# Optimization experiments

Hardware: AMD Instinct MI355X
Metric: run time of the kernel (lower is better)

## Reference

```python
import jax, jax.numpy as jnp
import numpy as np
from jax import lax

EPS = 1e-5  # flax BatchNorm default epsilon


def _conv(x, w, b, padding='SAME'):
    y = lax.conv_general_dilated(x, w, (1, 1), padding,
                                 dimension_numbers=('NHWC', 'HWIO', 'NHWC'))
    return y + b


def _maxpool(x, window, strides):
    return lax.reduce_window(x, -jnp.inf, lax.max,
                             (1,) + window + (1,), (1,) + strides + (1,), 'SAME')


def _bn_train(x, scale, bias):
    # training-mode BatchNorm: batch statistics over N,H,W
    m = x.mean(axis=(0, 1, 2))
    v = x.var(axis=(0, 1, 2))
    return (x - m) * lax.rsqrt(v + EPS) * scale + bias


def _lstm(x, wx, wh, b, carry, reverse):
    # x: (B, T, D); flax LSTMCell gate order i, f, g, o; bias lives on the
    # hidden dense in flax but is an equivalent single additive term here.
    xs = jnp.swapaxes(x @ wx + b, 0, 1)  # (T, B, 4H), input GEMM hoisted out of scan

    def step(ch, xt):
        c, h = ch
        g = xt + h @ wh
        i, f, gg, o = jnp.split(g, 4, axis=-1)
        c = jax.nn.sigmoid(f) * c + jax.nn.sigmoid(i) * jnp.tanh(gg)
        h = jax.nn.sigmoid(o) * jnp.tanh(c)
        return (c, h), h

    carry, ys = lax.scan(step, carry, xs, reverse=reverse)
    return carry, jnp.swapaxes(ys, 0, 1)  # (B, T, H)


def _forward(x, conv1_w, conv1_b, conv2_w, conv2_b, conv3_w, conv3_b, bn1_s, bn1_b,
             conv4_w, conv4_b, bn2_s, bn2_b, conv5_w, conv5_b, bn3_s, bn3_b,
             conv6_w, conv6_b, bn4_s, bn4_b, conv7_w, conv7_b, bn5_s, bn5_b,
             wq, bq, wk, bk, wv, bv,
             l1f_wx, l1f_wh, l1f_b, l1r_wx, l1r_wh, l1r_b,
             l2f_wx, l2f_wh, l2f_b, l2r_wx, l2r_wh, l2r_b, wo, bo):
    x = jax.nn.relu(_conv(x, conv1_w, conv1_b))
    x = _maxpool(x, (2, 2), (2, 2))
    x = jax.nn.relu(_conv(x, conv2_w, conv2_b))
    x = _maxpool(x, (2, 2), (2, 2))
    x = jax.nn.relu(_bn_train(_conv(x, conv3_w, conv3_b), bn1_s, bn1_b))
    x = jax.nn.relu(_bn_train(_conv(x, conv4_w, conv4_b), bn2_s, bn2_b))
    x = _maxpool(x, (2, 2), (1, 2))
    x = jax.nn.relu(_bn_train(_conv(x, conv5_w, conv5_b), bn3_s, bn3_b))
    x = jax.nn.relu(_bn_train(_conv(x, conv6_w, conv6_b), bn4_s, bn4_b))
    x = _maxpool(x, (2, 2), (1, 2))
    x = jax.nn.relu(_bn_train(_conv(x, conv7_w, conv7_b, padding='VALID'), bn5_s, bn5_b))
    B = x.shape[0]
    x = x.reshape(B, x.shape[1], -1)  # (B, T=H', W'*512); seq axis is height
    q = x @ wq + bq
    k = x @ wk + bk
    v = x @ wv + bv
    qk = jax.nn.softmax(jnp.einsum('btk,bsk->bts', q, k) / 32.0, axis=-1)
    x = jnp.einsum('btk,bts->bsk', v, qk)
    # stack 1: reverse LSTM deliberately starts from forward's FINAL carry (as in source)
    carry = (jnp.zeros((B, 256), x.dtype), jnp.zeros((B, 256), x.dtype))
    carry, y1 = _lstm(x, l1f_wx, l1f_wh, l1f_b, carry, reverse=False)
    carry, y2 = _lstm(x, l1r_wx, l1r_wh, l1r_b, carry, reverse=True)
    x1 = jnp.concatenate([y1, y2], axis=-1)
    # stack 2
    carry = (jnp.zeros((B, 512), x.dtype), jnp.zeros((B, 512), x.dtype))
    carry, y2b = _lstm(x1, l2f_wx, l2f_wh, l2f_b, carry, reverse=False)
    carry, y3 = _lstm(x1, l2r_wx, l2r_wh, l2r_b, carry, reverse=True)
    x = jnp.concatenate([y3, y2b], axis=-1)
    return x @ wo + bo


def setup_inputs() -> dict:
    key = jax.random.key(0)
    ks = iter(jax.random.split(key, 64))

    def cw(kh, kw, ci, co):
        return jax.random.normal(next(ks), (kh, kw, ci, co), jnp.float32) / np.float32(np.sqrt(kh * kw * ci))

    def dw(i, o):
        return jax.random.normal(next(ks), (i, o), jnp.float32) / np.float32(np.sqrt(i))

    z = lambda *s: jnp.zeros(s, jnp.float32)
    ones = lambda *s: jnp.ones(s, jnp.float32)
    class_nums = 1000
    d_in = 15 * 512  # W'=15 after conv stack, 512 channels
    inp = {
        'x': jax.random.normal(next(ks), (32, 64, 256, 3), jnp.float32),
        'conv1_w': cw(3, 3, 3, 64), 'conv1_b': z(64),
        'conv2_w': cw(3, 3, 64, 128), 'conv2_b': z(128),
        'conv3_w': cw(3, 3, 128, 256), 'conv3_b': z(256), 'bn1_s': ones(256), 'bn1_b': z(256),
        'conv4_w': cw(3, 3, 256, 256), 'conv4_b': z(256), 'bn2_s': ones(256), 'bn2_b': z(256),
        'conv5_w': cw(3, 3, 256, 512), 'conv5_b': z(512), 'bn3_s': ones(512), 'bn3_b': z(512),
        'conv6_w': cw(3, 3, 512, 512), 'conv6_b': z(512), 'bn4_s': ones(512), 'bn4_b': z(512),
        'conv7_w': cw(2, 2, 512, 512), 'conv7_b': z(512), 'bn5_s': ones(512), 'bn5_b': z(512),
        'wq': dw(d_in, 512), 'bq': z(512),
        'wk': dw(d_in, 512), 'bk': z(512),
        'wv': dw(d_in, 512), 'bv': z(512),
        'l1f_wx': dw(512, 4 * 256), 'l1f_wh': dw(256, 4 * 256), 'l1f_b': z(4 * 256),
        'l1r_wx': dw(512, 4 * 256), 'l1r_wh': dw(256, 4 * 256), 'l1r_b': z(4 * 256),
        'l2f_wx': dw(512, 4 * 512), 'l2f_wh': dw(512, 4 * 512), 'l2f_b': z(4 * 512),
        'l2r_wx': dw(512, 4 * 512), 'l2r_wh': dw(512, 4 * 512), 'l2r_b': z(4 * 512),
        'wo': dw(1024, class_nums), 'bo': z(class_nums),
    }
    return inp


def reference(x, conv1_w, conv1_b, conv2_w, conv2_b, conv3_w, conv3_b, bn1_s, bn1_b,
              conv4_w, conv4_b, bn2_s, bn2_b, conv5_w, conv5_b, bn3_s, bn3_b,
              conv6_w, conv6_b, bn4_s, bn4_b, conv7_w, conv7_b, bn5_s, bn5_b,
              wq, bq, wk, bk, wv, bv,
              l1f_wx, l1f_wh, l1f_b, l1r_wx, l1r_wh, l1r_b,
              l2f_wx, l2f_wh, l2f_b, l2r_wx, l2r_wh, l2r_b, wo, bo):
    return _forward(x, conv1_w, conv1_b, conv2_w, conv2_b, conv3_w, conv3_b, bn1_s, bn1_b,
                    conv4_w, conv4_b, bn2_s, bn2_b, conv5_w, conv5_b, bn3_s, bn3_b,
                    conv6_w, conv6_b, bn4_s, bn4_b, conv7_w, conv7_b, bn5_s, bn5_b,
                    wq, bq, wk, bk, wv, bv,
                    l1f_wx, l1f_wh, l1f_b, l1r_wx, l1r_wh, l1r_b,
                    l2f_wx, l2f_wh, l2f_b, l2r_wx, l2r_wh, l2r_b, wo, bo)
```

## Files before the change

kernel.cpp:

```cpp
#include <hip/hip_runtime.h>
#include <math.h>

#define DIV_UP(a,b) (((a)+(b)-1)/(b))

typedef _Float16 half_t;
typedef _Float16 half8 __attribute__((ext_vector_type(8)));
typedef float f32x4 __attribute__((ext_vector_type(4)));

#define FLAG_RELU   1
#define FLAG_OUTF32 2
#define FLAG_SPLITK 4
#define FLAG_ATOMIC 8
#define FLAG_BNSUMS 16

#define GLDS16(src, dst) \
  __builtin_amdgcn_global_load_lds((const __attribute__((address_space(1))) void*)(src), \
                                   (__attribute__((address_space(3))) void*)(dst), 16, 0, 0)

__device__ __forceinline__ float fsig_(float x){ return 1.0f/(1.0f+__expf(-x)); }
__device__ __forceinline__ float ftanh_(float x){
  float ax = fabsf(x);
  float e = __expf(-2.0f*ax);
  float t = (1.0f - e)/(1.0f + e);
  return copysignf(t, x);
}

struct TpAll {
  const float* src[14];
  half_t* dst[14];
  int K[14];
  int N[14];
  int prefix[15];
};

__global__ __launch_bounds__(256) void transpose_cvt_all_kernel(TpAll a)
{
  __shared__ float tile[32][33];
  int bid = blockIdx.x;
  int z = 0;
  while (bid >= a.prefix[z+1]) ++z;
  int local = bid - a.prefix[z];
  const float* w = a.src[z];
  half_t* wT = a.dst[z];
  int K = a.K[z], N = a.N[z];
  int tilesX = (N + 31) >> 5;
  int nt = (local % tilesX) * 32;
  int kt = (local / tilesX) * 32;
  int tx = threadIdx.x & 31, ty = threadIdx.x >> 5;
  #pragma unroll
  for (int r = 0; r < 4; ++r) {
    int k = kt + ty + r*8, n = nt + tx;
    tile[ty + r*8][tx] = (k < K && n < N) ? w[(long)k*N + n] : 0.f;
  }
  __syncthreads();
  #pragma unroll
  for (int r = 0; r < 4; ++r) {
    int n = nt + ty + r*8, k = kt + tx;
    if (n < N && k < K) wT[(long)n*K + k] = (half_t)tile[tx][ty + r*8];
  }
}

__global__ __launch_bounds__(256) void conv1_kernel(
    const float* __restrict__ x, const float* __restrict__ w,
    const float* __restrict__ bias, half_t* __restrict__ out)
{
  __shared__ float xs[3][258*3];
  int nb = blockIdx.x;
  int n = nb >> 6, ho = nb & 63;
  int tid = threadIdx.x;
  int co = tid & 63;
  float wreg[27];
  #pragma unroll
  for (int k = 0; k < 27; ++k) wreg[k] = w[k*64 + co];
  float bco = bias[co];
  for (int i = tid; i < 3*258*3; i += 256) {
    int row = i / (258*3); int rem = i % (258*3);
    int col = rem / 3;     int ci  = rem % 3;
    int ih = ho - 1 + row; int iw = col - 1;
    float v = 0.f;
    if (ih >= 0 && ih < 64 && iw >= 0 && iw < 256)
      v = x[(((long)n*64 + ih)*256 + iw)*3 + ci];
    xs[row][col*3 + ci] = v;
  }
  __syncthreads();
  int wave = tid >> 6;
  for (int p = 0; p < 64; ++p) {
    int wo = wave*64 + p;
    float acc = bco;
    #pragma unroll
    for (int kh = 0; kh < 3; ++kh)
      #pragma unroll
      for (int kw = 0; kw < 3; ++kw)
        #pragma unroll
        for (int ci = 0; ci < 3; ++ci)
          acc = fmaf(xs[kh][(wo+kw)*3 + ci], wreg[(kh*3+kw)*3 + ci], acc);
    acc = fmaxf(acc, 0.f);
    out[(((long)n*64 + ho)*256 + wo)*64 + co] = (half_t)acc;
  }
}

struct GOut { const half_t* wT; const float* bias; void* out; };

__global__ __launch_bounds__(256) void mfma_conv_kernel(
    const half_t* __restrict__ x, GOut g0, GOut g1, GOut g2,
    const half_t* __restrict__ zbuf, float* __restrict__ bns,
    int N,int H,int W,int Ci,int Ho,int Wo,int Co,
    int KH,int KW,int padH,int padW,
    int M,int K,int flags,int splitS)
{
  GOut g;
  int ciBeg = 0, ciEnd = Ci;
  if (flags & FLAG_SPLITK) {
    g = g0;
    int span = Ci / splitS;
    ciBeg = blockIdx.z * span;
    ciEnd = ciBeg + span;
  } else {
    g = (blockIdx.z == 0) ? g0 : (blockIdx.z == 1 ? g1 : g2);
  }
  const half_t* __restrict__ wT = g.wT;
  __shared__ half_t As[128*64];
  __shared__ half_t Bs[128*64];
  int tid = threadIdx.x;
  int m0 = blockIdx.y*128, n0 = blockIdx.x*128;
  int wave = tid >> 6, lane = tid & 63;
  int l15 = lane & 15, quad = lane >> 4;
  int x7 = lane & 7;
  int wm = (wave & 1) * 64, wn = (wave >> 1) * 64;

  int rSub = tid >> 3;
  int colHalf = (((tid & 7) ^ (rSub & 7))) * 8;

  int ho_[4], wo_[4], ni_[4]; bool av_[4];
  #pragma unroll
  for (int i = 0; i < 4; ++i) {
    int m = m0 + i*32 + rSub;
    av_[i] = m < M;
    int mm = av_[i] ? m : 0;
    wo_[i] = mm % Wo; int t2 = mm / Wo;
    ho_[i] = t2 % Ho; ni_[i] = t2 / Ho;
  }
  const half_t* bBase[4];
  #pragma unroll
  for (int i = 0; i < 4; ++i) {
    int n = n0 + i*32 + rSub;
    bBase[i] = (n < Co) ? (wT + (long)n*K + colHalf) : nullptr;
  }

  int pch0 = ((quad)     ^ x7) * 8;
  int pch1 = ((4 + quad) ^ x7) * 8;

  f32x4 acc[4][4];
  #pragma unroll
  for (int i = 0; i < 4; ++i)
    #pragma unroll
    for (int j = 0; j < 4; ++j)
      acc[i][j] = (f32x4){0.f, 0.f, 0.f, 0.f};

  int kg = ciBeg;
  for (int kh = 0; kh < KH; ++kh) {
    for (int kw = 0; kw < KW; ++kw) {
      long aOff[4]; bool aval[4];
      #pragma unroll
      for (int i = 0; i < 4; ++i) {
        int ih = ho_[i] - padH + kh, iw = wo_[i] - padW + kw;
        bool ok = av_[i] && ih >= 0 && ih < H && iw >= 0 && iw < W;
        aval[i] = ok;
        aOff[i] = ok ? ((((long)ni_[i]*H + ih)*W + iw)*(long)Ci + colHalf) : 0;
      }
      for (int ci = ciBeg; ci < ciEnd; ci += 64, kg += 64) {
        #pragma unroll
        for (int i = 0; i < 4; ++i) {
          const half_t* sa = aval[i] ? (x + aOff[i] + ci) : zbuf;
          GLDS16(sa, As + i*2048 + wave*512);
          const half_t* sb = bBase[i] ? (bBase[i] + kg) : zbuf;
          GLDS16(sb, Bs + i*2048 + wave*512);
        }
        __syncthreads();
        {
          half8 af[4], bf[4];
          #pragma unroll
          for (int i = 0; i < 4; ++i)
            af[i] = *reinterpret_cast<half8*>(&As[(wm + i*16 + l15)*64 + pch0]);
          #pragma unroll
          for (int j = 0; j < 4; ++j)
            bf[j] = *reinterpret_cast<half8*>(&Bs[(wn + j*16 + l15)*64 + pch0]);
          #pragma unroll
          for (int i = 0; i < 4; ++i)
            #pragma unroll
            for (int j = 0; j < 4; ++j)
              acc[i][j] = __builtin_amdgcn_mfma_f32_16x16x32_f16(af[i], bf[j], acc[i][j], 0, 0, 0);
        }
        {
          half8 af[4], bf[4];
          #pragma unroll
          for (int i = 0; i < 4; ++i)
            af[i] = *reinterpret_cast<half8*>(&As[(wm + i*16 + l15)*64 + pch1]);
          #pragma unroll
          for (int j = 0; j < 4; ++j)
            bf[j] = *reinterpret_cast<half8*>(&Bs[(wn + j*16 + l15)*64 + pch1]);
          #pragma unroll
          for (int i = 0; i < 4; ++i)
            #pragma unroll
            for (int j = 0; j < 4; ++j)
              acc[i][j] = __builtin_amdgcn_mfma_f32_16x16x32_f16(af[i], bf[j], acc[i][j], 0, 0, 0);
        }
        __syncthreads();
      }
    }
  }

  if (flags & FLAG_BNSUMS) {
    float* red = (float*)As;
    #pragma unroll
    for (int j = 0; j < 4; ++j) {
      int n = n0 + wn + j*16 + l15;
      float bv = g.bias[n];
      float s = 0.f, q = 0.f;
      #pragma unroll
      for (int i = 0; i < 4; ++i)
        #pragma unroll
        for (int r = 0; r < 4; ++r) {
          int m = m0 + wm + i*16 + quad*4 + r;
          if (m < M) { float v = acc[i][j][r] + bv; s += v; q += v*v; }
        }
      int idx = ((((wave*4 + quad)*16 + l15)*4) + j)*2;
      red[idx] = s; red[idx+1] = q;
    }
    __syncthreads();
    if (tid < 128) {
      int hi = tid >> 6;
      int jj = (tid >> 4) & 3, ll = tid & 15;
      float s = 0.f, q = 0.f;
      #pragma unroll
      for (int w2 = 0; w2 < 2; ++w2)
        #pragma unroll
        for (int qd = 0; qd < 4; ++qd) {
          int idx = (((((hi*2 + w2)*4 + qd)*16 + ll)*4) + jj)*2;
          s += red[idx]; q += red[idx+1];
        }
      int n = n0 + tid;
      atomicAdd(&bns[n], s);
      atomicAdd(&bns[Co + n], q);
    }
  }

  #pragma unroll
  for (int i = 0; i < 4; ++i) {
    #pragma unroll
    for (int r = 0; r < 4; ++r) {
      int m = m0 + wm + i*16 + quad*4 + r;
      if (m >= M) continue;
      #pragma unroll
      for (int j = 0; j < 4; ++j) {
        int n = n0 + wn + j*16 + l15;
        if (n >= Co) continue;
        if (flags & FLAG_ATOMIC) {
          atomicAdd(&((float*)g.out)[(long)m*Co + n], acc[i][j][r]);
        } else {
          float v = acc[i][j][r] + g.bias[n];
          if (flags & FLAG_RELU) v = fmaxf(v, 0.f);
          if (flags & FLAG_OUTF32) ((float*)g.out)[(long)m*Co + n] = v;
          else ((half_t*)g.out)[(long)m*Co + n] = (half_t)v;
        }
      }
    }
  }
}

__global__ __launch_bounds__(256) void maxpool8_kernel(
    const half_t* __restrict__ x, half_t* __restrict__ out,
    int N,int H,int W,int C,int Ho,int Wo,int sH,int sW)
{
  int C8 = C >> 3;
  long idx = (long)blockIdx.x*256 + threadIdx.x;
  long total8 = (long)N*Ho*Wo*C8;
  if (idx >= total8) return;
  int cb = (int)(idx % C8);
  long pix = idx / C8;
  int wo = (int)(pix % Wo); long t2 = pix / Wo;
  int ho = (int)(t2 % Ho); int n = (int)(t2 / Ho);
  int c = cb * 8;
  float m[8];
  #pragma unroll
  for (int e = 0; e < 8; ++e) m[e] = -INFINITY;
  for (int i = 0; i < 2; ++i) {
    int ih = ho*sH + i;
    if (ih >= H) continue;
    for (int j = 0; j < 2; ++j) {
      int iw = wo*sW + j;
      if (iw >= W) continue;
      half8 v = *reinterpret_cast<const half8*>(x + (((long)n*H + ih)*W + iw)*C + c);
      #pragma unroll
      for (int e = 0; e < 8; ++e) m[e] = fmaxf(m[e], (float)v[e]);
    }
  }
  half8 o;
  #pragma unroll
  for (int e = 0; e < 8; ++e) o[e] = (half_t)m[e];
  *reinterpret_cast<half8*>(out + idx*8) = o;
}

__global__ __launch_bounds__(256) void bn_apply_relu8_kernel(
    half_t* __restrict__ x, const float* __restrict__ sums,
    const float* __restrict__ scale, const float* __restrict__ bias,
    long total8, int C, float invN)
{
  long idx = (long)blockIdx.x*256 + threadIdx.x;
  if (idx >= total8) return;
  int c = (int)((idx*8) % C);
  half8 v = *reinterpret_cast<half8*>(x + idx*8);
  half8 o;
  #pragma unroll
  for (int e = 0; e < 8; ++e) {
    float mean = sums[c+e] * invN;
    float var  = sums[C + c+e] * invN - mean*mean;
    float rstd = rsqrtf(var + 1e-5f);
    float y = ((float)v[e] - mean) * rstd * scale[c+e] + bias[c+e];
    o[e] = (half_t)fmaxf(y, 0.0f);
  }
  *reinterpret_cast<half8*>(x + idx*8) = o;
}

__global__ __launch_bounds__(256) void bn_pool8_kernel(
    const half_t* __restrict__ x, half_t* __restrict__ out,
    const float* __restrict__ sums, const float* __restrict__ scale,
    const float* __restrict__ bias,
    int N,int H,int W,int C,int Ho,int Wo,int sH,int sW, float invN)
{
  int C8 = C >> 3;
  long idx = (long)blockIdx.x*256 + threadIdx.x;
  long total8 = (long)N*Ho*Wo*C8;
  if (idx >= total8) return;
  int cb = (int)(idx % C8);
  long pix = idx / C8;
  int wo = (int)(pix % Wo); long t2 = pix / Wo;
  int ho = (int)(t2 % Ho); int n = (int)(t2 / Ho);
  int c = cb * 8;
  float mean[8], rs[8], bb[8];
  #pragma unroll
  for (int e = 0; e < 8; ++e) {
    mean[e] = sums[c+e] * invN;
    float var = sums[C + c+e] * invN - mean[e]*mean[e];
    rs[e] = rsqrtf(var + 1e-5f) * scale[c+e];
    bb[e] = bias[c+e];
  }
  float m[8];
  #pragma unroll
  for (int e = 0; e < 8; ++e) m[e] = -INFINITY;
  for (int i = 0; i < 2; ++i) {
    int ih = ho*sH + i;
    if (ih >= H) continue;
    for (int j = 0; j < 2; ++j) {
      int iw = wo*sW + j;
      if (iw >= W) continue;
      half8 v = *reinterpret_cast<const half8*>(x + (((long)n*H + ih)*W + iw)*C + c);
      #pragma unroll
      for (int e = 0; e < 8; ++e) {
        float y = fmaxf(((float)v[e] - mean[e]) * rs[e] + bb[e], 0.f);
        m[e] = fmaxf(m[e], y);
      }
    }
  }
  half8 o;
  #pragma unroll
  for (int e = 0; e < 8; ++e) o[e] = (half_t)m[e];
  *reinterpret_cast<half8*>(out + idx*8) = o;
}

__global__ __launch_bounds__(256) void bias_fill_kernel(
    float* __restrict__ out, const float* __restrict__ b0,
    const float* __restrict__ b1, const float* __restrict__ b2, int total)
{
  int idx = blockIdx.x*256 + threadIdx.x;
  if (idx >= total) return;
  int n = idx % 1536;
  float v = (n < 512) ? b0[n] : (n < 1024 ? b1[n-512] : b2[n-1024]);
  out[idx] = v;
}

__global__ __launch_bounds__(256) void attention_kernel(
    const float* __restrict__ qkv, half_t* __restrict__ out,
    int T, int D, int ld)
{
  int b = blockIdx.x;
  int tid = threadIdx.x;
  __shared__ float P[15][16];
  if (tid < T*T) {
    int t = tid / T, s = tid % T;
    const float* qp = qkv + ((long)b*T + t)*ld;
    const float* kp = qkv + ((long)b*T + s)*ld + 512;
    float acc = 0.f;
    for (int d = 0; d < D; d += 4) {
      float4 qv = *reinterpret_cast<const float4*>(qp + d);
      float4 kv = *reinterpret_cast<const float4*>(kp + d);
      acc += qv.x*kv.x + qv.y*kv.y + qv.z*kv.z + qv.w*kv.w;
    }
    P[t][s] = acc * (1.0f/32.0f);
  }
  __syncthreads();
  if (tid < T) {
    float mx = -INFINITY;
    for (int s = 0; s < T; ++s) mx = fmaxf(mx, P[tid][s]);
    float sum = 0.f;
    for (int s = 0; s < T; ++s) { float e = expf(P[tid][s] - mx); P[tid][s] = e; sum += e; }
    float inv = 1.0f / sum;
    for (int s = 0; s < T; ++s) P[tid][s] *= inv;
  }
  __syncthreads();
  for (int idx = tid; idx < T*D; idx += 256) {
    int s = idx / D, kk2 = idx % D;
    float acc = 0.f;
    #pragma unroll
    for (int t = 0; t < 15; ++t)
      acc += qkv[((long)b*T + t)*ld + 1024 + kk2] * P[t][s];
    out[((long)b*T + s)*D + kk2] = (half_t)acc;
  }
}

#define MAXK 512
#define HSROW (MAXK + 8)

template<int N64, int HLOG>
__device__ __forceinline__ void stage_h(
    const unsigned long long* __restrict__ src, half_t (*hs)[HSROW], int tid)
{
  unsigned long long tmp[N64];
  #pragma unroll
  for (int u = 0; u < N64; ++u)
    tmp[u] = __hip_atomic_load(src + tid + u*256, __ATOMIC_RELAXED, __HIP_MEMORY_SCOPE_AGENT);
  #pragma unroll
  for (int u = 0; u < N64; ++u) {
    int idx = tid + u*256;
    int row = idx >> (HLOG - 2);
    int col = (idx & ((1 << (HLOG - 2)) - 1)) * 4;
    *reinterpret_cast<unsigned long long*>(&hs[row][col]) = tmp[u];
  }
}

__global__ __launch_bounds__(256, 1) void lstm_persistent_kernel(
    const float* __restrict__ preF, const float* __restrict__ preR,
    const float* __restrict__ whF, const float* __restrict__ whR,
    half_t* __restrict__ hbuf, half_t* __restrict__ y,
    int* __restrict__ flags, int H, int nblk,
    int ystride, int yoffF, int yoffR)
{
  __shared__ half_t BsT[64][HSROW];
  __shared__ half_t hs[32][HSROW];
  __shared__ float gates[32][65];
  int tid = threadIdx.x;
  int jb0 = blockIdx.x * 16;
  int H4 = 4 * H;
  int lane = tid & 63, wave = tid >> 6;
  int l15 = lane & 15, quad = lane >> 4;
  int bb = tid >> 3;
  int jj0 = (tid & 7) * 2;

  float cst[2] = {0.f, 0.f};

  for (int idx = tid; idx < H*64; idx += 256) {
    int k = idx >> 6, c = idx & 63;
    int g = c >> 4, jj = c & 15;
    BsT[c][k] = (half_t)whF[(long)k*H4 + g*H + jb0 + jj];
  }
  const float* pre = preF;
  int yoff = yoffF;
  __syncthreads();

  for (int s = 0; s < 30; ++s) {
    if (s == 15) {
      __syncthreads();
      for (int idx = tid; idx < H*64; idx += 256) {
        int k = idx >> 6, c = idx & 63;
        int g = c >> 4, jj = c & 15;
        BsT[c][k] = (half_t)whR[(long)k*H4 + g*H + jb0 + jj];
      }
      pre = preR; yoff = yoffR;
      __syncthreads();
    }
    int t = (s < 15) ? s : 29 - s;

    float pv[8];
    {
      const float* pp = pre + (long)(bb*15 + t)*H4 + jb0 + jj0;
      #pragma unroll
      for (int p = 0; p < 2; ++p) {
        pv[p*4+0] = pp[p];
        pv[p*4+1] = pp[H + p];
        pv[p*4+2] = pp[2*H + p];
        pv[p*4+3] = pp[3*H + p];
      }
    }

    const unsigned long long* hsrc =
        (const unsigned long long*)(hbuf + (long)(s & 1) * 32 * H);
    if (H == 512) stage_h<16, 9>(hsrc, hs, tid);
    else          stage_h<8, 8>(hsrc, hs, tid);
    __syncthreads();

    f32x4 acc0 = {0.f,0.f,0.f,0.f}, acc1 = {0.f,0.f,0.f,0.f};
    for (int k0 = 0; k0 < H; k0 += 32) {
      half8 bf = *reinterpret_cast<half8*>(&BsT[wave*16 + l15][k0 + quad*8]);
      half8 a0 = *reinterpret_cast<half8*>(&hs[l15][k0 + quad*8]);
      half8 a1 = *reinterpret_cast<half8*>(&hs[16 + l15][k0 + quad*8]);
      acc0 = __builtin_amdgcn_mfma_f32_16x16x32_f16(a0, bf, acc0, 0, 0, 0);
      acc1 = __builtin_amdgcn_mfma_f32_16x16x32_f16(a1, bf, acc1, 0, 0, 0);
    }
    #pragma unroll
    for (int r = 0; r < 4; ++r) {
      gates[quad*4 + r][wave*16 + l15]      = acc0[r];
      gates[16 + quad*4 + r][wave*16 + l15] = acc1[r];
    }
    __syncthreads();

    unsigned hpack;
    {
      half_t hn2[2];
      #pragma unroll
      for (int p = 0; p < 2; ++p) {
        int jj = jj0 + p;
        float gi = pv[p*4+0] + gates[bb][jj];
        float gf = pv[p*4+1] + gates[bb][16 + jj];
        float gg = pv[p*4+2] + gates[bb][32 + jj];
        float go = pv[p*4+3] + gates[bb][48 + jj];
        gi = fsig_(gi); gf = fsig_(gf); gg = ftanh_(gg); go = fsig_(go);
        float cn = gf * cst[p] + gi * gg;
        cst[p] = cn;
        hn2[p] = (half_t)(go * ftanh_(cn));
      }
      hpack = *reinterpret_cast<unsigned*>(hn2);
      half_t* hdst = hbuf + (long)((s + 1) & 1) * 32 * H;
      __hip_atomic_store((unsigned*)(hdst + (long)bb*H + jb0 + jj0), hpack,
                         __ATOMIC_RELAXED, __HIP_MEMORY_SCOPE_AGENT);
    }

    if (s < 29) {
      __syncthreads();
      if (tid == 0)
        __hip_atomic_store(&flags[blockIdx.x*16], s + 1,
                           __ATOMIC_RELAXED, __HIP_MEMORY_SCOPE_AGENT);
      *reinterpret_cast<unsigned*>(&y[(long)(bb*15 + t)*ystride + yoff + jb0 + jj0]) = hpack;
      if (tid < 64) {
        int target = s + 1;
        for (;;) {
          int vv = (tid < nblk)
            ? __hip_atomic_load(&flags[tid*16], __ATOMIC_RELAXED, __HIP_MEMORY_SCOPE_AGENT)
            : target;
          if (__all(vv >= target)) break;
          __builtin_amdgcn_s_sleep(1);
        }
      }
      __syncthreads();
    } else {
      *reinterpret_cast<unsigned*>(&y[(long)(bb*15 + t)*ystride + yoff + jb0 + jj0]) = hpack;
    }
  }
}

extern "C" void kernel_launch(void* const* d_in, const int* in_sizes, int n_in,
                              void* d_out, int out_size, void* d_ws, size_t ws_size,
                              hipStream_t stream)
{
  const float* x       = (const float*)d_in[0];
  const float* c1w     = (const float*)d_in[1];  const float* c1b = (const float*)d_in[2];
  const float* c2w     = (const float*)d_in[3];  const float* c2b = (const float*)d_in[4];
  const float* c3w     = (const float*)d_in[5];  const float* c3b = (const float*)d_in[6];
  const float* bn1s    = (const float*)d_in[7];  const float* bn1b = (const float*)d_in[8];
  const float* c4w     = (const float*)d_in[9];  const float* c4b = (const float*)d_in[10];
  const float* bn2s    = (const float*)d_in[11]; const float* bn2b = (const float*)d_in[12];
  const float* c5w     = (const float*)d_in[13]; const float* c5b = (const float*)d_in[14];
  const float* bn3s    = (const float*)d_in[15]; const float* bn3b = (const float*)d_in[16];
  const float* c6w     = (const float*)d_in[17]; const float* c6b = (const float*)d_in[18];
  const float* bn4s    = (const float*)d_in[19]; const float* bn4b = (const float*)d_in[20];
  const float* c7w     = (const float*)d_in[21]; const float* c7b = (const float*)d_in[22];
  const float* bn5s    = (const float*)d_in[23]; const float* bn5b = (const float*)d_in[24];
  const float* wq      = (const float*)d_in[25]; const float* bq = (const float*)d_in[26];
  const float* wk      = (const float*)d_in[27]; const float* bk = (const float*)d_in[28];
  const float* wv      = (const float*)d_in[29]; const float* bv = (const float*)d_in[30];
  const float* l1f_wx  = (const float*)d_in[31]; const float* l1f_wh = (const float*)d_in[32]; const float* l1f_b = (const float*)d_in[33];
  const float* l1r_wx  = (const float*)d_in[34]; const float* l1r_wh = (const float*)d_in[35]; const float* l1r_b = (const float*)d_in[36];
  const float* l2f_wx  = (const float*)d_in[37]; const float* l2f_wh = (const float*)d_in[38]; const float* l2f_b = (const float*)d_in[39];
  const float* l2r_wx  = (const float*)d_in[40]; const float* l2r_wh = (const float*)d_in[41]; const float* l2r_b = (const float*)d_in[42];
  const float* wo      = (const float*)d_in[43]; const float* bo = (const float*)d_in[44];
  float* outp = (float*)d_out;

  char* base = (char*)d_ws;
  half_t* actA = (half_t*)base;
  half_t* actB = (half_t*)(base + 67108864);
  half_t* wtA  = (half_t*)(base + 100663296);
  float*  f32a = (float*)(base + 143687680);
  half_t* h16a = (half_t*)(base + 158736384);

  half_t* wt2  = wtA;
  half_t* wt3  = wtA + 73728;
  half_t* wt4  = wtA + 368640;
  half_t* wt5  = wtA + 958464;
  half_t* wt6  = wtA + 2138112;
  half_t* wt7  = wtA + 4497408;
  half_t* wtq  = wtA + 5545984;
  half_t* wtk  = wtA + 9478144;
  half_t* wtv  = wtA + 13410304;
  half_t* wt1f = wtA + 17342464;
  half_t* wt1r = wtA + 17866752;
  half_t* wt2f = wtA + 18391040;
  half_t* wt2r = wtA + 19439616;
  half_t* wto  = wtA + 20488192;

  float* qkvbuf = f32a;
  float* pre1f = f32a + 737280;
  float* pre1r = f32a + 1228800;
  float* pre2f = f32a + 1720320;
  float* pre2r = f32a + 2703360;

  half_t* ao  = h16a;
  half_t* x1  = h16a + 245760;
  half_t* x2  = h16a + 491520;
  half_t* hb1 = h16a + 983040;
  half_t* hb2 = hb1 + 16384;
  int*    flags1 = (int*)(hb2 + 32768);
  int*    flags2 = flags1 + 512;
  half_t* zbuf   = (half_t*)(flags2 + 512);
  float*  bnz    = (float*)(zbuf + 32);

  auto convm = [&](const half_t* in, const half_t* wt, const float* b, void* out,
                   int N,int H,int W,int Ci,int Ho,int Wo,int Co,
                   int KH,int KW,int pH,int pW,int flags, float* bns){
    int M = N*Ho*Wo, K = KH*KW*Ci;
    dim3 grid(DIV_UP(Co,128), DIV_UP(M,128), 1);
    GOut g{wt, b, out};
    mfma_conv_kernel<<<grid,256,0,stream>>>(in,g,g,g,zbuf,bns,N,H,W,Ci,Ho,Wo,Co,
                                            KH,KW,pH,pW,M,K,flags,1);
  };
  auto gemm3 = [&](const half_t* A, GOut g0, GOut g1, GOut g2, int nz,
                   int M, int Nn, int K, int flags, int splitS){
    dim3 grid(DIV_UP(Nn,128), DIV_UP(M,128), nz);
    mfma_conv_kernel<<<grid,256,0,stream>>>(A,g0,g1,g2,zbuf,bnz,M,1,1,K,1,1,Nn,
                                            1,1,0,0,M,K,flags,splitS);
  };
  auto pool = [&](const half_t* in, half_t* out, int N,int H,int W,int C,
                  int Ho,int Wo,int sH,int sW){
    long total8 = (long)N*Ho*Wo*(C/8);
    maxpool8_kernel<<<(int)DIV_UP(total8,256),256,0,stream>>>(in,out,N,H,W,C,Ho,Wo,sH,sW);
  };
  auto bnApply = [&](half_t* buf, long nPix, int C, const float* s, const float* b,
                     float* sums){
    long total8 = nPix * C / 8;
    bn_apply_relu8_kernel<<<(int)DIV_UP(total8,256),256,0,stream>>>(buf, sums, s, b, total8, C, 1.0f/(float)nPix);
  };
  auto bnPool = [&](const half_t* in, half_t* out, int N,int H,int W,int C,
                    int Ho,int Wo,int sH,int sW, long nPix,
                    const float* s, const float* b, float* sums){
    long total8 = (long)N*Ho*Wo*(C/8);
    bn_pool8_kernel<<<(int)DIV_UP(total8,256),256,0,stream>>>(
        in,out,sums,s,b,N,H,W,C,Ho,Wo,sH,sW,1.0f/(float)nPix);
  };

  hipMemsetAsync(hb1, 0, 143424, stream);

  {
    TpAll tp;
    const float* srcs[14] = {c2w,c3w,c4w,c5w,c6w,c7w,wq,wk,wv,l1f_wx,l1r_wx,l2f_wx,l2r_wx,wo};
    half_t* dsts[14] = {wt2,wt3,wt4,wt5,wt6,wt7,wtq,wtk,wtv,wt1f,wt1r,wt2f,wt2r,wto};
    int Ks[14] = {576,1152,2304,2304,4608,2048,7680,7680,7680,512,512,512,512,1024};
    int Ns[14] = {128,256,256,512,512,512,512,512,512,1024,1024,2048,2048,1000};
    int acc = 0;
    for (int i = 0; i < 14; ++i) {
      tp.src[i] = srcs[i]; tp.dst[i] = dsts[i]; tp.K[i] = Ks[i]; tp.N[i] = Ns[i];
      tp.prefix[i] = acc;
      acc += DIV_UP(Ks[i],32) * DIV_UP(Ns[i],32);
    }
    tp.prefix[14] = acc;
    transpose_cvt_all_kernel<<<acc,256,0,stream>>>(tp);
  }

  conv1_kernel<<<2048,256,0,stream>>>(x, c1w, c1b, actA);
  pool(actA, actB, 32,64,256,64,  32,128, 2,2);
  convm(actB, wt2, c2b, actA, 32,32,128,64,  32,128,128, 3,3,1,1, FLAG_RELU, bnz);
  pool(actA, actB, 32,32,128,128, 16,64, 2,2);
  convm(actB, wt3, c3b, actA, 32,16,64,128,  16,64,256,  3,3,1,1, FLAG_BNSUMS, bnz);
  bnApply(actA, 32768, 256, bn1s, bn1b, bnz);
  convm(actA, wt4, c4b, actB, 32,16,64,256,  16,64,256,  3,3,1,1, FLAG_BNSUMS, bnz + 2048);
  bnPool(actB, actA, 32,16,64,256, 16,32, 1,2, 32768, bn2s, bn2b, bnz + 2048);
  convm(actA, wt5, c5b, actB, 32,16,32,256,  16,32,512,  3,3,1,1, FLAG_BNSUMS, bnz + 4096);
  bnApply(actB, 16384, 512, bn3s, bn3b, bnz + 4096);
  convm(actB, wt6, c6b, actA, 32,16,32,512,  16,32,512,  3,3,1,1, FLAG_BNSUMS, bnz + 6144);
  bnPool(actA, actB, 32,16,32,512, 16,16, 1,2, 16384, bn4s, bn4b, bnz + 6144);
  convm(actB, wt7, c7b, actA, 32,16,16,512,  15,15,512,  2,2,0,0, FLAG_BNSUMS, bnz + 8192);
  bnApply(actA, 7200, 512, bn5s, bn5b, bnz + 8192);

  bias_fill_kernel<<<DIV_UP(480*1536,256),256,0,stream>>>(qkvbuf, bq, bk, bv, 480*1536);
  gemm3(actA, GOut{wtq, nullptr, qkvbuf}, GOut{wtq, nullptr, qkvbuf},
        GOut{wtq, nullptr, qkvbuf}, 4, 480, 1536, 7680, FLAG_SPLITK|FLAG_ATOMIC, 4);
  attention_kernel<<<32,256,0,stream>>>(qkvbuf, ao, 15, 512, 1536);

  gemm3(ao, GOut{wt1f, l1f_b, pre1f}, GOut{wt1r, l1r_b, pre1r},
        GOut{wt1r, l1r_b, pre1r}, 2, 480, 1024, 512, FLAG_OUTF32, 1);
  lstm_persistent_kernel<<<16,256,0,stream>>>(
      pre1f, pre1r, l1f_wh, l1r_wh, hb1, x1, flags1, 256, 16, 512, 0, 256);

  gemm3(x1, GOut{wt2f, l2f_b, pre2f}, GOut{wt2r, l2r_b, pre2r},
        GOut{wt2r, l2r_b, pre2r}, 2, 480, 2048, 512, FLAG_OUTF32, 1);
  lstm_persistent_kernel<<<32,256,0,stream>>>(
      pre2f, pre2r, l2f_wh, l2r_wh, hb2, x2, flags2, 512, 32, 1024, 512, 0);

  gemm3(x2, GOut{wto, bo, outp}, GOut{wto, bo, outp}, GOut{wto, bo, outp}, 1,
        480, 1000, 1024, FLAG_OUTF32, 1);
}
```

Before: 1.133 ms.

## Keep LSTM recurrent weights in registers and halve persistent block count

The persistent LSTM kernel now holds each wave's slice of the recurrent weight matrix in VGPRs (half8 arrays) rather than in LDS, and each block covers 32 hidden units instead of 16, so half as many blocks take part in the per-step grid barrier. Hidden size becomes a template parameter so the K loop fully unrolls. Flags are packed contiguously, the spin-wait sleep is removed, and pre-activation loads and h stores are widened to vectors. In exchange, register pressure rises sharply (up to 32 half8 per thread for H=512), which could cause spills, and each block does twice the MFMA work per step.

```diff
diff --git a/kernel.cpp b/kernel.cpp
--- a/kernel.cpp
+++ b/kernel.cpp
@@ -438,121 +438,131 @@
   }
 }
 
+template<int H>
 __global__ __launch_bounds__(256, 1) void lstm_persistent_kernel(
     const float* __restrict__ preF, const float* __restrict__ preR,
     const float* __restrict__ whF, const float* __restrict__ whR,
     half_t* __restrict__ hbuf, half_t* __restrict__ y,
-    int* __restrict__ flags, int H, int nblk,
+    int* __restrict__ flags, int nblk,
     int ystride, int yoffF, int yoffR)
 {
-  __shared__ half_t BsT[64][HSROW];
+  constexpr int KI = H / 32;
+  constexpr int H4 = 4 * H;
   __shared__ half_t hs[32][HSROW];
-  __shared__ float gates[32][65];
+  __shared__ float gates[32][133];
   int tid = threadIdx.x;
-  int jb0 = blockIdx.x * 16;
-  int H4 = 4 * H;
+  int jb0 = blockIdx.x * 32;
   int lane = tid & 63, wave = tid >> 6;
   int l15 = lane & 15, quad = lane >> 4;
   int bb = tid >> 3;
-  int jj0 = (tid & 7) * 2;
-
-  float cst[2] = {0.f, 0.f};
-
-  for (int idx = tid; idx < H*64; idx += 256) {
-    int k = idx >> 6, c = idx & 63;
-    int g = c >> 4, jj = c & 15;
-    BsT[c][k] = (half_t)whF[(long)k*H4 + g*H + jb0 + jj];
-  }
+  int jj0 = (tid & 7) * 4;
+
+  float cst[4] = {0.f, 0.f, 0.f, 0.f};
+  half8 wreg[2][KI];
+
+  auto loadw = [&](const float* __restrict__ wh) {
+    #pragma unroll
+    for (int f = 0; f < 2; ++f) {
+      int col = wave*H + jb0 + f*16 + l15;
+      #pragma unroll
+      for (int i = 0; i < KI; ++i) {
+        half8 v;
+        #pragma unroll
+        for (int e = 0; e < 8; ++e)
+          v[e] = (half_t)wh[(long)(i*32 + quad*8 + e)*H4 + col];
+        wreg[f][i] = v;
+      }
+    }
+  };
+
+  loadw(whF);
   const float* pre = preF;
   int yoff = yoffF;
-  __syncthreads();
 
   for (int s = 0; s < 30; ++s) {
     if (s == 15) {
-      __syncthreads();
-      for (int idx = tid; idx < H*64; idx += 256) {
-        int k = idx >> 6, c = idx & 63;
-        int g = c >> 4, jj = c & 15;
-        BsT[c][k] = (half_t)whR[(long)k*H4 + g*H + jb0 + jj];
-      }
+      loadw(whR);
       pre = preR; yoff = yoffR;
-      __syncthreads();
     }
     int t = (s < 15) ? s : 29 - s;
 
-    float pv[8];
+    float pv[16];
     {
       const float* pp = pre + (long)(bb*15 + t)*H4 + jb0 + jj0;
       #pragma unroll
-      for (int p = 0; p < 2; ++p) {
-        pv[p*4+0] = pp[p];
-        pv[p*4+1] = pp[H + p];
-        pv[p*4+2] = pp[2*H + p];
-        pv[p*4+3] = pp[3*H + p];
+      for (int g = 0; g < 4; ++g) {
+        f32x4 v = *reinterpret_cast<const f32x4*>(pp + g*H);
+        pv[g*4+0] = v[0]; pv[g*4+1] = v[1]; pv[g*4+2] = v[2]; pv[g*4+3] = v[3];
       }
     }
 
     const unsigned long long* hsrc =
         (const unsigned long long*)(hbuf + (long)(s & 1) * 32 * H);
-    if (H == 512) stage_h<16, 9>(hsrc, hs, tid);
-    else          stage_h<8, 8>(hsrc, hs, tid);
+    if constexpr (H == 512) stage_h<16, 9>(hsrc, hs, tid);
+    else                    stage_h<8, 8>(hsrc, hs, tid);
     __syncthreads();
 
-    f32x4 acc0 = {0.f,0.f,0.f,0.f}, acc1 = {0.f,0.f,0.f,0.f};
-    for (int k0 = 0; k0 < H; k0 += 32) {
-      half8 bf = *reinterpret_cast<half8*>(&BsT[wave*16 + l15][k0 + quad*8]);
-      half8 a0 = *reinterpret_cast<half8*>(&hs[l15][k0 + quad*8]);
-      half8 a1 = *reinterpret_cast<half8*>(&hs[16 + l15][k0 + quad*8]);
-      acc0 = __builtin_amdgcn_mfma_f32_16x16x32_f16(a0, bf, acc0, 0, 0, 0);
-      acc1 = __builtin_amdgcn_mfma_f32_16x16x32_f16(a1, bf, acc1, 0, 0, 0);
+    f32x4 acc00 = {0.f,0.f,0.f,0.f}, acc10 = {0.f,0.f,0.f,0.f};
+    f32x4 acc01 = {0.f,0.f,0.f,0.f}, acc11 = {0.f,0.f,0.f,0.f};
+    #pragma unroll
+    for (int i = 0; i < KI; ++i) {
+      half8 a0 = *reinterpret_cast<half8*>(&hs[l15][i*32 + quad*8]);
+      half8 a1 = *reinterpret_cast<half8*>(&hs[16 + l15][i*32 + quad*8]);
+      acc00 = __builtin_amdgcn_mfma_f32_16x16x32_f16(a0, wreg[0][i], acc00, 0, 0, 0);
+      acc10 = __builtin_amdgcn_mfma_f32_16x16x32_f16(a1, wreg[0][i], acc10, 0, 0, 0);
+      acc01 = __builtin_amdgcn_mfma_f32_16x16x32_f16(a0, wreg[1][i], acc01, 0, 0, 0);
+      acc11 = __builtin_amdgcn_mfma_f32_16x16x32_f16(a1, wreg[1][i], acc11, 0, 0, 0);
     }
     #pragma unroll
     for (int r = 0; r < 4; ++r) {
-      gates[quad*4 + r][wave*16 + l15]      = acc0[r];
-      gates[16 + quad*4 + r][wave*16 + l15] = acc1[r];
+      gates[quad*4 + r][wave*32 + l15]           = acc00[r];
+      gates[16 + quad*4 + r][wave*32 + l15]      = acc10[r];
+      gates[quad*4 + r][wave*32 + 16 + l15]      = acc01[r];
+      gates[16 + quad*4 + r][wave*32 + 16 + l15] = acc11[r];
     }
     __syncthreads();
 
-    unsigned hpack;
+    unsigned long long hpack;
     {
-      half_t hn2[2];
-      #pragma unroll
-      for (int p = 0; p < 2; ++p) {
-        int jj = jj0 + p;
-        float gi = pv[p*4+0] + gates[bb][jj];
-        float gf = pv[p*4+1] + gates[bb][16 + jj];
-        float gg = pv[p*4+2] + gates[bb][32 + jj];
-        float go = pv[p*4+3] + gates[bb][48 + jj];
+      half_t hn[4];
+      #pragma unroll
+      for (int p = 0; p < 4; ++p) {
+        int j = jj0 + p;
+        float gi = pv[p]      + gates[bb][j];
+        float gf = pv[4 + p]  + gates[bb][32 + j];
+        float gg = pv[8 + p]  + gates[bb][64 + j];
+        float go = pv[12 + p] + gates[bb][96 + j];
         gi = fsig_(gi); gf = fsig_(gf); gg = ftanh_(gg); go = fsig_(go);
         float cn = gf * cst[p] + gi * gg;
         cst[p] = cn;
-        hn2[p] = (half_t)(go * ftanh_(cn));
+        hn[p] = (half_t)(go * ftanh_(cn));
       }
-      hpack = *reinterpret_cast<unsigned*>(hn2);
+      hpack = *reinterpret_cast<unsigned long long*>(hn);
       half_t* hdst = hbuf + (long)((s + 1) & 1) * 32 * H;
-      __hip_atomic_store((unsigned*)(hdst + (long)bb*H + jb0 + jj0), hpack,
+      __hip_atomic_store((unsigned long long*)(hdst + (long)bb*H + jb0 + jj0), hpack,
                          __ATOMIC_RELAXED, __HIP_MEMORY_SCOPE_AGENT);
     }
 
     if (s < 29) {
       __syncthreads();
       if (tid == 0)
-        __hip_atomic_store(&flags[blockIdx.x*16], s + 1,
+        __hip_atomic_store(&flags[blockIdx.x], s + 1,
                            __ATOMIC_RELAXED, __HIP_MEMORY_SCOPE_AGENT);
-      *reinterpret_cast<unsigned*>(&y[(long)(bb*15 + t)*ystride + yoff + jb0 + jj0]) = hpack;
+      *reinterpret_cast<unsigned long long*>(
+          &y[(long)(bb*15 + t)*ystride + yoff + jb0 + jj0]) = hpack;
       if (tid < 64) {
         int target = s + 1;
         for (;;) {
           int vv = (tid < nblk)
-            ? __hip_atomic_load(&flags[tid*16], __ATOMIC_RELAXED, __HIP_MEMORY_SCOPE_AGENT)
+            ? __hip_atomic_load(&flags[tid], __ATOMIC_RELAXED, __HIP_MEMORY_SCOPE_AGENT)
             : target;
           if (__all(vv >= target)) break;
-          __builtin_amdgcn_s_sleep(1);
         }
       }
       __syncthreads();
     } else {
-      *reinterpret_cast<unsigned*>(&y[(long)(bb*15 + t)*ystride + yoff + jb0 + jj0]) = hpack;
+      *reinterpret_cast<unsigned long long*>(
+          &y[(long)(bb*15 + t)*ystride + yoff + jb0 + jj0]) = hpack;
     }
   }
 }
@@ -695,13 +705,13 @@
 
   gemm3(ao, GOut{wt1f, l1f_b, pre1f}, GOut{wt1r, l1r_b, pre1r},
         GOut{wt1r, l1r_b, pre1r}, 2, 480, 1024, 512, FLAG_OUTF32, 1);
-  lstm_persistent_kernel<<<16,256,0,stream>>>(
-      pre1f, pre1r, l1f_wh, l1r_wh, hb1, x1, flags1, 256, 16, 512, 0, 256);
+  lstm_persistent_kernel<256><<<8,256,0,stream>>>(
+      pre1f, pre1r, l1f_wh, l1r_wh, hb1, x1, flags1, 8, 512, 0, 256);
 
   gemm3(x1, GOut{wt2f, l2f_b, pre2f}, GOut{wt2r, l2r_b, pre2r},
         GOut{wt2r, l2r_b, pre2r}, 2, 480, 2048, 512, FLAG_OUTF32, 1);
-  lstm_persistent_kernel<<<32,256,0,stream>>>(
-      pre2f, pre2r, l2f_wh, l2r_wh, hb2, x2, flags2, 512, 32, 1024, 512, 0);
+  lstm_persistent_kernel<512><<<16,256,0,stream>>>(
+      pre2f, pre2r, l2f_wh, l2r_wh, hb2, x2, flags2, 16, 1024, 512, 0);
 
   gemm3(x2, GOut{wto, bo, outp}, GOut{wto, bo, outp}, GOut{wto, bo, outp}, 1,
         480, 1000, 1024, FLAG_OUTF32, 1);
```

Measured after the change: 1.172 ms. 1.03x slower.
